# Kernel tuning notes

Measured on AMD Instinct MI355X. Metric: run time of the kernel, lower is better.

Reference implementation:

```python
import jax, jax.numpy as jnp
import numpy as np

G = 64          # graphs in batch
P = 31          # original nodes per graph
N_ORIG = G * P  # 1984 original nodes
N = N_ORIG + G  # 2048 total nodes (one virtual node per graph, appended at end)
D = 512         # hidden_dim
H = 8           # num_heads
DK = D // H     # per-head dim
FF = 2048       # dim_ff
L = 4           # num_layers
NF = 32         # num_node_features
MAX_SP = 100
MAX_DEG = 100


def setup_inputs() -> dict:
    key = jax.random.key(0)
    ks = jax.random.split(key, 24)
    s = 0.02
    return {
        "x": jax.random.normal(ks[0], (N_ORIG, NF), jnp.float32),
        "sp_matrix": jax.random.randint(ks[1], (N_ORIG, N_ORIG), 0, MAX_SP + 1, jnp.int32),
        "batch_ids": jnp.concatenate([
            jnp.repeat(jnp.arange(G, dtype=jnp.int32), P),
            jnp.arange(G, dtype=jnp.int32),
        ]),
        "degrees": jax.random.randint(ks[2], (N,), 0, MAX_DEG + 1, jnp.int32),
        "init_W": jax.random.normal(ks[3], (NF, D), jnp.float32) * s,
        "init_b": jnp.zeros((D,), jnp.float32),
        "cent_emb": jax.random.normal(ks[4], (MAX_DEG + 1, D), jnp.float32) * s,
        "dist_biases": jax.random.normal(ks[5], (MAX_SP + 2,), jnp.float32) * s,
        "virt_bias": jnp.zeros((), jnp.float32),
        "Wq": jax.random.normal(ks[6], (L, H, D, DK), jnp.float32) * s,
        "bq": jnp.zeros((L, H, DK), jnp.float32),
        "Wk": jax.random.normal(ks[7], (L, H, D, DK), jnp.float32) * s,
        "bk": jnp.zeros((L, H, DK), jnp.float32),
        "Wv": jax.random.normal(ks[8], (L, H, D, DK), jnp.float32) * s,
        "bv": jnp.zeros((L, H, DK), jnp.float32),
        "Wo": jax.random.normal(ks[9], (L, D, D), jnp.float32) * s,
        "bo": jnp.zeros((L, D), jnp.float32),
        "W1": jax.random.normal(ks[10], (L, D, FF), jnp.float32) * s,
        "b1": jnp.zeros((L, FF), jnp.float32),
        "W2": jax.random.normal(ks[11], (L, FF, D), jnp.float32) * s,
        "b2": jnp.zeros((L, D), jnp.float32),
    }


def _ln(h):
    # F.layer_norm with no affine params, eps=1e-5
    m = jnp.mean(h, axis=-1, keepdims=True)
    v = jnp.var(h, axis=-1, keepdims=True)
    return (h - m) / jnp.sqrt(v + 1e-5)


def reference(x, sp_matrix, batch_ids, degrees,
              init_W, init_b, cent_emb, dist_biases, virt_bias,
              Wq, bq, Wk, bk, Wv, bv, Wo, bo, W1, b1, W2, b2):
    same = batch_ids[:, None] == batch_ids[None, :]          # attention mask [N, N]
    is_virt = jnp.arange(N) >= N_ORIG

    # B matrix: fill with last distance bias (detached: torch uses .item()),
    # overwrite orig-orig block with sp-distance biases, virtual edges with
    # virt_bias, diagonal with dist_biases[0].
    fill = jax.lax.stop_gradient(dist_biases[-1])
    B = jnp.full((N, N), fill, dtype=jnp.float32)
    sp = jnp.minimum(sp_matrix, MAX_SP)
    B = B.at[:N_ORIG, :N_ORIG].set(dist_biases[sp])
    ve = (is_virt[:, None] ^ is_virt[None, :]) & same        # virt<->non-virt, same graph
    B = jnp.where(ve, virt_bias, B)
    diag = jnp.arange(N)
    B = B.at[diag, diag].set(dist_biases[0])

    # init projection, append virtual node states, add centrality encoding
    h = x @ init_W + init_b                                  # [N_ORIG, D]
    h = jnp.concatenate([h, jnp.zeros((G, D), h.dtype)], axis=0)   # [N, D]
    h = h + cent_emb[jnp.minimum(degrees, MAX_DEG)]

    scale = 1.0 / jnp.sqrt(jnp.float32(DK))
    for l in range(L):
        hn = _ln(h)
        Q = jnp.einsum('nd,hdk->hnk', hn, Wq[l]) + bq[l][:, None, :]   # [H, N, DK]
        K = jnp.einsum('nd,hdk->hnk', hn, Wk[l]) + bk[l][:, None, :]
        V = jnp.einsum('nd,hdk->hnk', hn, Wv[l]) + bv[l][:, None, :]
        logits = jnp.einsum('hik,hjk->hij', Q, K) * scale + B          # [H, N, N]
        logits = jnp.where(same, logits, -jnp.inf)
        w = jax.nn.softmax(logits, axis=-1)
        o = jnp.einsum('hij,hjk->hik', w, V)                           # [H, N, DK]
        o = jnp.transpose(o, (1, 0, 2)).reshape(N, D)                  # concat heads
        h = o @ Wo[l] + bo[l] + h                                      # residual
        hn2 = _ln(h)
        h = h + jax.nn.relu(hn2 @ W1[l] + b1[l]) @ W2[l] + b2[l]       # FFN residual

    return h[N_ORIG:]   # virtual node states, [G, D]
```

## Files before the change

### kernel.cpp

```cpp
#include <hip/hip_runtime.h>


#define NG   64
#define NP   31
#define NORI 1984
#define NT   2048
#define DIM  512
#define NHD  8
#define DKH  64
#define FFD  2048
#define NLAY 4
#define NFEA 32

typedef __attribute__((ext_vector_type(8))) short short8;
typedef __attribute__((ext_vector_type(4))) float floatx4;

__device__ __forceinline__ unsigned short f2bf(float f) {
    union { float f; unsigned u; } v; v.f = f;
    unsigned r = v.u + 0x7fffu + ((v.u >> 16) & 1u);
    return (unsigned short)(r >> 16);
}
__device__ __forceinline__ float bf2f(unsigned short u) {
    union { unsigned u; float f; } v; v.u = ((unsigned)u) << 16;
    return v.f;
}

__global__ __launch_bounds__(256) void prep_all(
    const float* __restrict__ x, const int* __restrict__ degrees,
    const float* __restrict__ init_W, const float* __restrict__ init_b,
    const float* __restrict__ cent_emb, float* __restrict__ h,
    const int* __restrict__ sp, const float* __restrict__ db,
    const float* __restrict__ virt_bias, float* __restrict__ Bg,
    const float* __restrict__ Wq, const float* __restrict__ Wk,
    const float* __restrict__ Wv, const float* __restrict__ bq,
    const float* __restrict__ bk, const float* __restrict__ bv,
    unsigned short* __restrict__ Wqkv_t, float* __restrict__ bqkv,
    const float* __restrict__ Wo, const float* __restrict__ W1,
    const float* __restrict__ W2, unsigned short* __restrict__ Wo_t,
    unsigned short* __restrict__ W1_t, unsigned short* __restrict__ W2_t)
{
    __shared__ float tl[32][33];
    int u = blockIdx.x;
    int tid = threadIdx.x;

    if (u < 2112) {
        int n = u;
        if (n >= NT) {
            int g = n - NT;
            float vb = virt_bias[0];
            for (int e = tid; e < 1024; e += 256) {
                int i = e >> 5, j = e & 31;
                float v;
                if (i == j) v = db[0];
                else if (i < NP && j < NP) {
                    int s = sp[(size_t)(g * NP + i) * NORI + g * NP + j];
                    v = db[s < 100 ? s : 100];
                } else v = vb;
                Bg[(size_t)g * 1024 + e] = v;
            }
            return;
        }
        float* xs = &tl[0][0];
        if (n < NORI && tid < NFEA) xs[tid] = x[(size_t)n * NFEA + tid];
        __syncthreads();
        int deg = degrees[n]; if (deg > 100) deg = 100;
        for (int d = tid; d < DIM; d += 256) {
            float v = cent_emb[(size_t)deg * DIM + d];
            if (n < NORI) {
                float acc = init_b[d];
                #pragma unroll
                for (int k = 0; k < NFEA; ++k) acc += xs[k] * init_W[(size_t)k * DIM + d];
                v += acc;
            }
            h[(size_t)n * DIM + d] = v;
        }
        return;
    }
    if (u < 5208) {
        int tile = u - 2112;
        if (tile >= 3072) {
            int idx = (tile - 3072) * 256 + tid;
            if (idx < NLAY * 1536) {
                int l = idx / 1536, c = idx % 1536;
                int which = c >> 9, cc = c & 511;
                const float* b = (which == 0) ? bq : (which == 1) ? bk : bv;
                bqkv[idx] = b[(size_t)l * 512 + cc];
            }
            return;
        }
        int slice = tile >> 5;
        int tloc = tile & 31;
        int dt = tloc >> 1, kt = tloc & 1;
        int l = slice / 24; int rem = slice % 24; int which = rem >> 3; int hh = rem & 7;
        const float* W = (which == 0) ? Wq : (which == 1) ? Wk : Wv;
        const float* in = W + (size_t)(l * 8 + hh) * DIM * DKH;
        int tr = tid >> 5, tc = tid & 31;
        #pragma unroll
        for (int pp = 0; pp < 4; ++pp)
            tl[tr + pp * 8][tc] = in[(size_t)(dt * 32 + tr + pp * 8) * DKH + kt * 32 + tc];
        __syncthreads();
        unsigned short* out = Wqkv_t +
            ((size_t)l * 1536 + which * 512 + hh * 64 + kt * 32) * DIM + dt * 32;
        #pragma unroll
        for (int pp = 0; pp < 4; ++pp)
            out[(size_t)(tr + pp * 8) * DIM + tc] = f2bf(tl[tc][tr + pp * 8]);
        return;
    }
    {
        int id = u - 5208;
        const float* in; unsigned short* outp; int R, C, l, rt, ct;
        if (id < 1024) {
            l = id >> 8; int t = id & 255; rt = t >> 4; ct = t & 15;
            in = Wo; outp = Wo_t; R = 512; C = 512;
        } else if (id < 5120) {
            int t2 = id - 1024; l = t2 >> 10; int t = t2 & 1023; rt = t >> 6; ct = t & 63;
            in = W1; outp = W1_t; R = 512; C = 2048;
        } else {
            int t2 = id - 5120; l = t2 >> 10; int t = t2 & 1023; rt = t >> 4; ct = t & 15;
            in = W2; outp = W2_t; R = 2048; C = 512;
        }
        const float* ip = in + (size_t)l * R * C;
        unsigned short* op = outp + (size_t)l * R * C;
        int r0 = rt * 32, c0 = ct * 32;
        int tr = tid >> 5, tc = tid & 31;
        #pragma unroll
        for (int pp = 0; pp < 4; ++pp)
            tl[tr + pp * 8][tc] = ip[(size_t)(r0 + tr + pp * 8) * C + c0 + tc];
        __syncthreads();
        #pragma unroll
        for (int pp = 0; pp < 4; ++pp)
            op[(size_t)(c0 + tr + pp * 8) * R + r0 + tc] = f2bf(tl[tc][tr + pp * 8]);
    }
}

__global__ __launch_bounds__(256) void layernorm_bf16(
    const float* __restrict__ in, unsigned short* __restrict__ out, int row0,
    float* __restrict__ fout)
{
    int n = row0 + blockIdx.x;
    int tid = threadIdx.x;
    const float* row = in + (size_t)n * DIM;
    float v0 = row[tid], v1 = row[tid + 256];
    float s = v0 + v1;
    float sq = v0 * v0 + v1 * v1;
    #pragma unroll
    for (int off = 32; off > 0; off >>= 1) {
        s  += __shfl_down(s, off);
        sq += __shfl_down(sq, off);
    }
    __shared__ float red[8];
    int wave = tid >> 6;
    if ((tid & 63) == 0) { red[wave] = s; red[4 + wave] = sq; }
    __syncthreads();
    float ts  = red[0] + red[1] + red[2] + red[3];
    float tsq = red[4] + red[5] + red[6] + red[7];
    float m   = ts * (1.0f / DIM);
    float var = tsq * (1.0f / DIM) - m * m;
    float inv = rsqrtf(var + 1e-5f);
    out[(size_t)n * DIM + tid]       = f2bf((v0 - m) * inv);
    out[(size_t)n * DIM + tid + 256] = f2bf((v1 - m) * inv);
    if (fout) {
        fout[(size_t)(n - row0) * DIM + tid]       = v0;
        fout[(size_t)(n - row0) * DIM + tid + 256] = v1;
    }
}

template<int SPLITK>
__global__ __launch_bounds__(256) void gemm64(
    const unsigned short* __restrict__ A, const unsigned short* __restrict__ Bt,
    const float* __restrict__ bias, void* __restrict__ out,
    int Nfull, int K, int moff, int flags, int P, int C, int orow)
{
    __shared__ __align__(16) unsigned short Asl[64 * 72];
    __shared__ __align__(16) unsigned short Bsl[64 * 72];
    int id = blockIdx.x;
    int by, bx, bz;
    if (P >= 8) {
        int xcd = id & 7, t = id >> 3, G = P >> 3;
        by = xcd + 8 * (t % G);
        int r2 = t / G;
        bx = r2 % C;
        bz = r2 / C;
    } else {
        by = id % P; int r2 = id / P; bx = r2 % C; bz = r2 / C;
    }
    int tid = threadIdx.x;
    int row0 = moff + by * 64, col0 = bx * 64;
    if ((flags & 4) && col0 < 512 && row0 < NORI) return;
    int kslice = K / SPLITK;
    int kbeg = bz * kslice;
    int wave = tid >> 6, lane = tid & 63;
    int quad = lane >> 4, m16 = lane & 15;
    int mw = (wave >> 1) * 32, nw = (wave & 1) * 32;
    floatx4 acc[2][2] = {};
    for (int k0 = kbeg; k0 < kbeg + kslice; k0 += 64) {
        #pragma unroll
        for (int p = 0; p < 2; ++p) {
            int idx = (p * 256 + tid) * 8;
            int r = idx >> 6, kk = idx & 63;
            *(float4*)(Asl + r * 72 + kk) =
                *(const float4*)(A + (size_t)(row0 + r) * K + k0 + kk);
            *(float4*)(Bsl + r * 72 + kk) =
                *(const float4*)(Bt + (size_t)(col0 + r) * K + k0 + kk);
        }
        __syncthreads();
        #pragma unroll
        for (int ks = 0; ks < 64; ks += 32) {
            short8 a[2], b[2];
            #pragma unroll
            for (int mi = 0; mi < 2; ++mi)
                a[mi] = *(const short8*)(Asl + (mw + mi * 16 + m16) * 72 + ks + quad * 8);
            #pragma unroll
            for (int ni = 0; ni < 2; ++ni)
                b[ni] = *(const short8*)(Bsl + (nw + ni * 16 + m16) * 72 + ks + quad * 8);
            #pragma unroll
            for (int mi = 0; mi < 2; ++mi)
                #pragma unroll
                for (int ni = 0; ni < 2; ++ni)
                    acc[mi][ni] = __builtin_amdgcn_mfma_f32_16x16x32_bf16(
                        a[mi], b[ni], acc[mi][ni], 0, 0, 0);
        }
        __syncthreads();
    }
    if (SPLITK == 1) {
        int do_relu = flags & 1, out_bf = flags & 2;
        #pragma unroll
        for (int mi = 0; mi < 2; ++mi) {
            #pragma unroll
            for (int ni = 0; ni < 2; ++ni) {
                int col = col0 + nw + ni * 16 + m16;
                float bval = bias[col];
                #pragma unroll
                for (int rr = 0; rr < 4; ++rr) {
                    int row = row0 + mw + mi * 16 + quad * 4 + rr;
                    float v = acc[mi][ni][rr] + bval;
                    if (do_relu) v = fmaxf(v, 0.0f);
                    if (out_bf) ((unsigned short*)out)[(size_t)(row - orow) * Nfull + col] = f2bf(v);
                    else        ((float*)out)[(size_t)(row - orow) * Nfull + col] = v;
                }
            }
        }
    } else {
        float* o = (float*)out;
        float bscale = (bz == 0) ? 1.0f : 0.0f;
        #pragma unroll
        for (int mi = 0; mi < 2; ++mi) {
            #pragma unroll
            for (int ni = 0; ni < 2; ++ni) {
                int col = col0 + nw + ni * 16 + m16;
                float bval = bias[col] * bscale;
                #pragma unroll
                for (int rr = 0; rr < 4; ++rr) {
                    int row = row0 + mw + mi * 16 + quad * 4 + rr;
                    atomicAdd(&o[(size_t)(row - orow) * Nfull + col],
                              acc[mi][ni][rr] + bval);
                }
            }
        }
    }
}

template<int SPLITK>
__global__ __launch_bounds__(256) void gemm128(
    const unsigned short* __restrict__ A, const unsigned short* __restrict__ Bt,
    const float* __restrict__ bias, void* __restrict__ out,
    int Nfull, int K, int flags, int P, int C)
{
    __shared__ __align__(16) unsigned short Asl[128 * 64];
    __shared__ __align__(16) unsigned short Bsl[128 * 64];
    int id = blockIdx.x;
    int xcd = id & 7, t = id >> 3, Gp = P >> 3;
    int by = xcd + 8 * (t % Gp);
    int r2 = t / Gp;
    int bx = r2 % C;
    int bz = r2 / C;
    int tid = threadIdx.x;
    int row0 = by * 128, col0 = bx * 128;
    if ((flags & 4) && col0 < 512 && row0 + 128 <= NORI) return;
    int kslice = K / SPLITK;
    int kbeg = bz * kslice;
    int wave = tid >> 6, lane = tid & 63;
    int quad = lane >> 4, m16 = lane & 15;
    int mw = (wave >> 1) * 64, nw = (wave & 1) * 64;
    int lr = lane >> 3;
    int srcswz = ((lane & 7) ^ lr) << 3;
    int rdswz = (m16 & 7) << 4;
    const unsigned short* Abase = A + (size_t)row0 * K;
    const unsigned short* Bbase = Bt + (size_t)col0 * K;
    floatx4 acc[4][4] = {};
    for (int k0 = kbeg; k0 < kbeg + kslice; k0 += 64) {
        #pragma unroll
        for (int p = 0; p < 4; ++p) {
            int chunk = wave * 4 + p;
            int r = chunk * 8 + lr;
            __builtin_amdgcn_global_load_lds(
                (const __attribute__((address_space(1))) unsigned int*)
                    (Abase + (size_t)r * K + k0 + srcswz),
                (__attribute__((address_space(3))) unsigned int*)
                    (Asl + chunk * 512 + lane * 8), 16, 0, 0);
            __builtin_amdgcn_global_load_lds(
                (const __attribute__((address_space(1))) unsigned int*)
                    (Bbase + (size_t)r * K + k0 + srcswz),
                (__attribute__((address_space(3))) unsigned int*)
                    (Bsl + chunk * 512 + lane * 8), 16, 0, 0);
        }
        __syncthreads();
        #pragma unroll
        for (int ks = 0; ks < 64; ks += 32) {
            short8 a[4], b[4];
            int cb = (ks + quad * 8) * 2;
            #pragma unroll
            for (int mi = 0; mi < 4; ++mi)
                a[mi] = *(const short8*)((const char*)Asl +
                        (mw + mi * 16 + m16) * 128 + (cb ^ rdswz));
            #pragma unroll
            for (int ni = 0; ni < 4; ++ni)
                b[ni] = *(const short8*)((const char*)Bsl +
                        (nw + ni * 16 + m16) * 128 + (cb ^ rdswz));
            #pragma unroll
            for (int mi = 0; mi < 4; ++mi)
                #pragma unroll
                for (int ni = 0; ni < 4; ++ni)
                    acc[mi][ni] = __builtin_amdgcn_mfma_f32_16x16x32_bf16(
                        a[mi], b[ni], acc[mi][ni], 0, 0, 0);
        }
        __syncthreads();
    }
    if (SPLITK == 1) {
        int do_relu = flags & 1, out_bf = flags & 2;
        #pragma unroll
        for (int mi = 0; mi < 4; ++mi) {
            #pragma unroll
            for (int ni = 0; ni < 4; ++ni) {
                int col = col0 + nw + ni * 16 + m16;
                float bval = bias[col];
                #pragma unroll
                for (int rr = 0; rr < 4; ++rr) {
                    int row = row0 + mw + mi * 16 + quad * 4 + rr;
                    float v = acc[mi][ni][rr] + bval;
                    if (do_relu) v = fmaxf(v, 0.0f);
                    if (out_bf) ((unsigned short*)out)[(size_t)row * Nfull + col] = f2bf(v);
                    else        ((float*)out)[(size_t)row * Nfull + col] = v;
                }
            }
        }
    } else {
        float* o = (float*)out;
        float bscale = (bz == 0) ? 1.0f : 0.0f;
        #pragma unroll
        for (int mi = 0; mi < 4; ++mi) {
            #pragma unroll
            for (int ni = 0; ni < 4; ++ni) {
                int col = col0 + nw + ni * 16 + m16;
                float bval = bias[col] * bscale;
                #pragma unroll
                for (int rr = 0; rr < 4; ++rr) {
                    int row = row0 + mw + mi * 16 + quad * 4 + rr;
                    atomicAdd(&o[(size_t)row * Nfull + col], acc[mi][ni][rr] + bval);
                }
            }
        }
    }
}

__global__ __launch_bounds__(256) void attention(
    const unsigned short* __restrict__ qkv,
    const float* __restrict__ Bg,
    unsigned short* __restrict__ O)
{
    int g = blockIdx.x >> 3;
    int hh = blockIdx.x & 7;
    __shared__ float Qs[32][65], Ks[32][65], Vs[32][65];
    __shared__ float S[32][33];
    int tid = threadIdx.x;
    int i = tid >> 3;
    int c0 = (tid & 7) * 8;
    int gn = (i < NP) ? g * NP + i : NORI + g;
    const unsigned short* base = qkv + (size_t)gn * 1536 + hh * DKH;
    short8 qv = *(const short8*)(base + c0);
    short8 kv = *(const short8*)(base + 512 + c0);
    short8 vv = *(const short8*)(base + 1024 + c0);
    #pragma unroll
    for (int j = 0; j < 8; ++j) {
        Qs[i][c0 + j] = bf2f((unsigned short)qv[j]);
        Ks[i][c0 + j] = bf2f((unsigned short)kv[j]);
        Vs[i][c0 + j] = bf2f((unsigned short)vv[j]);
    }
    __syncthreads();
    const float scale = 0.125f;
    #pragma unroll
    for (int e = 0; e < 4; ++e) {
        int idx = tid + e * 256;
        int si = idx >> 5, sj = idx & 31;
        float dot = 0.0f;
        #pragma unroll
        for (int k = 0; k < DKH; ++k) dot += Qs[si][k] * Ks[sj][k];
        S[si][sj] = dot * scale + Bg[(size_t)g * 1024 + si * 32 + sj];
    }
    __syncthreads();
    if (tid < 32) {
        float mx = -1e30f;
        #pragma unroll
        for (int j = 0; j < 32; ++j) mx = fmaxf(mx, S[tid][j]);
        float sum = 0.0f;
        #pragma unroll
        for (int j = 0; j < 32; ++j) { float e = __expf(S[tid][j] - mx); S[tid][j] = e; sum += e; }
        float inv = 1.0f / sum;
        #pragma unroll
        for (int j = 0; j < 32; ++j) S[tid][j] *= inv;
    }
    __syncthreads();
    short8 ov;
    #pragma unroll
    for (int cc = 0; cc < 8; ++cc) {
        float acc = 0.0f;
        #pragma unroll
        for (int j = 0; j < 32; ++j) acc += S[i][j] * Vs[j][c0 + cc];
        ov[cc] = (short)f2bf(acc);
    }
    *(short8*)(O + (size_t)gn * DIM + hh * DKH + c0) = ov;
}

__global__ __launch_bounds__(64) void attention_last(
    const unsigned short* __restrict__ qkv, const float* __restrict__ Bg,
    unsigned short* __restrict__ O)
{
    int g = blockIdx.x >> 3, hh = blockIdx.x & 7;
    __shared__ float Ks[32][65], Vs[32][65];
    __shared__ float Qs[64], P[32];
    int tid = threadIdx.x;
    int j = tid & 31, hf = tid >> 5;
    int gn = (j < NP) ? g * NP + j : NORI + g;
    const unsigned short* kb = qkv + (size_t)gn * 1536 + hh * DKH + 512 + hf * 32;
    #pragma unroll
    for (int c = 0; c < 32; c += 8) {
        short8 k8 = *(const short8*)(kb + c);
        short8 v8 = *(const short8*)(kb + 512 + c);
        #pragma unroll
        for (int t = 0; t < 8; ++t) {
            Ks[j][hf * 32 + c + t] = bf2f((unsigned short)k8[t]);
            Vs[j][hf * 32 + c + t] = bf2f((unsigned short)v8[t]);
        }
    }
    Qs[tid] = bf2f(qkv[(size_t)(NORI + g) * 1536 + hh * DKH + tid]);
    __syncthreads();
    float s;
    if (tid < 32) {
        float dot = 0.0f;
        #pragma unroll
        for (int k = 0; k < 64; ++k) dot += Qs[k] * Ks[tid][k];
        s = dot * 0.125f + Bg[(size_t)g * 1024 + 31 * 32 + tid];
    } else s = -1e30f;
    float mx = s;
    #pragma unroll
    for (int off = 32; off > 0; off >>= 1) mx = fmaxf(mx, __shfl_xor(mx, off));
    float e = (tid < 32) ? __expf(s - mx) : 0.0f;
    float sum = e;
    #pragma unroll
    for (int off = 32; off > 0; off >>= 1) sum += __shfl_xor(sum, off);
    if (tid < 32) P[tid] = e / sum;
    __syncthreads();
    float acc = 0.0f;
    #pragma unroll
    for (int jj = 0; jj < 32; ++jj) acc += P[jj] * Vs[jj][tid];
    O[(size_t)(NORI + g) * DIM + hh * DKH + tid] = f2bf(acc);
}

extern "C" void kernel_launch(void* const* d_in, const int* in_sizes, int n_in,
                              void* d_out, int out_size, void* d_ws, size_t ws_size,
                              hipStream_t stream)
{
    const float* x        = (const float*)d_in[0];
    const int*   sp       = (const int*)d_in[1];
    const int*   degrees  = (const int*)d_in[3];
    const float* init_W   = (const float*)d_in[4];
    const float* init_b   = (const float*)d_in[5];
    const float* cent_emb = (const float*)d_in[6];
    const float* db       = (const float*)d_in[7];
    const float* vbias    = (const float*)d_in[8];
    const float* Wq       = (const float*)d_in[9];
    const float* bq       = (const float*)d_in[10];
    const float* Wk       = (const float*)d_in[11];
    const float* bk       = (const float*)d_in[12];
    const float* Wv       = (const float*)d_in[13];
    const float* bv       = (const float*)d_in[14];
    const float* Wo       = (const float*)d_in[15];
    const float* bo       = (const float*)d_in[16];
    const float* W1       = (const float*)d_in[17];
    const float* b1       = (const float*)d_in[18];
    const float* W2       = (const float*)d_in[19];
    const float* b2       = (const float*)d_in[20];

    char* ws = (char*)d_ws;
    float*          h      = (float*)ws;          ws += (size_t)NT * DIM * 4;
    unsigned short* hn     = (unsigned short*)ws; ws += (size_t)NT * DIM * 2;
    unsigned short* o      = (unsigned short*)ws; ws += (size_t)NT * DIM * 2;
    unsigned short* qkv    = (unsigned short*)ws; ws += (size_t)NT * FFD * 2;
    float*          Bg     = (float*)ws;          ws += (size_t)NG * 1024 * 4;
    unsigned short* Wqkv_t = (unsigned short*)ws; ws += (size_t)NLAY * 1536 * DIM * 2;
    unsigned short* Wo_t   = (unsigned short*)ws; ws += (size_t)NLAY * DIM * DIM * 2;
    unsigned short* W1_t   = (unsigned short*)ws; ws += (size_t)NLAY * FFD * DIM * 2;
    unsigned short* W2_t   = (unsigned short*)ws; ws += (size_t)NLAY * DIM * FFD * 2;
    float*          bqkv   = (float*)ws;          ws += (size_t)NLAY * 1536 * 4;
    unsigned short* ffnb   = qkv;

    prep_all<<<14424, 256, 0, stream>>>(
        x, degrees, init_W, init_b, cent_emb, h, sp, db, vbias, Bg,
        Wq, Wk, Wv, bq, bk, bv, Wqkv_t, bqkv, Wo, W1, W2, Wo_t, W1_t, W2_t);

    for (int l = 0; l < NLAY - 1; ++l) {
        layernorm_bf16<<<NT, 256, 0, stream>>>(h, hn, 0, nullptr);
        gemm128<1><<<16 * 12, 256, 0, stream>>>(
            hn, Wqkv_t + (size_t)l * 1536 * DIM, bqkv + (size_t)l * 1536,
            qkv, 1536, DIM, 2, 16, 12);
        attention<<<NG * NHD, 256, 0, stream>>>(qkv, Bg, o);
        gemm128<2><<<16 * 4 * 2, 256, 0, stream>>>(
            o, Wo_t + (size_t)l * DIM * DIM, bo + (size_t)l * DIM,
            h, DIM, DIM, 0, 16, 4);
        layernorm_bf16<<<NT, 256, 0, stream>>>(h, hn, 0, nullptr);
        gemm128<1><<<16 * 16, 256, 0, stream>>>(
            hn, W1_t + (size_t)l * FFD * DIM, b1 + (size_t)l * FFD,
            ffnb, FFD, DIM, 3, 16, 16);
        gemm128<4><<<16 * 4 * 4, 256, 0, stream>>>(
            ffnb, W2_t + (size_t)l * DIM * FFD, b2 + (size_t)l * DIM,
            h, DIM, FFD, 0, 16, 4);
    }

    {
        int l = NLAY - 1;
        layernorm_bf16<<<NT, 256, 0, stream>>>(h, hn, 0, nullptr);
        gemm128<1><<<16 * 12, 256, 0, stream>>>(
            hn, Wqkv_t + (size_t)l * 1536 * DIM, bqkv + (size_t)l * 1536,
            qkv, 1536, DIM, 6, 16, 12);
        attention_last<<<NG * NHD, 64, 0, stream>>>(qkv, Bg, o);
        gemm64<8><<<1 * 8 * 8, 256, 0, stream>>>(
            o, Wo_t + (size_t)l * DIM * DIM, bo + (size_t)l * DIM,
            h, DIM, DIM, NORI, 0, 1, 8, 0);
        layernorm_bf16<<<NG, 256, 0, stream>>>(h, hn, NORI, (float*)d_out);
        gemm64<1><<<1 * 32, 256, 0, stream>>>(
            hn, W1_t + (size_t)l * FFD * DIM, b1 + (size_t)l * FFD,
            ffnb, FFD, DIM, NORI, 3, 1, 32, 0);
        gemm64<8><<<1 * 8 * 8, 256, 0, stream>>>(
            ffnb, W2_t + (size_t)l * DIM * FFD, b2 + (size_t)l * DIM,
            d_out, DIM, FFD, NORI, 0, 1, 8, NORI);
    }
}
```

Measured before the change: 452.5 us.

## Double-buffer LDS tiles in gemm128 and raise Wo split-K to four

The GEMM main loop now keeps two LDS buffers and issues the global-to-LDS loads for the next K tile before computing on the current one. Explicit vmcnt waits and raw barriers replace the previous syncthreads pair, so memory latency can overlap the MFMA work. Shared memory per block doubles, which may reduce occupancy. The Wo projection also moves from split-K 2 to 4, giving more blocks but more atomic adds into h.

```diff
diff --git a/kernel.cpp b/kernel.cpp
--- a/kernel.cpp
+++ b/kernel.cpp
@@ -260,14 +260,36 @@
     }
 }
 
+__device__ __forceinline__ void stage128(
+    const unsigned short* __restrict__ Abase, const unsigned short* __restrict__ Bbase,
+    int K, int k0, unsigned short* Asl, unsigned short* Bsl,
+    int wave, int lane, int lr, int scol)
+{
+    #pragma unroll
+    for (int p = 0; p < 4; ++p) {
+        int chunk = wave * 4 + p;
+        int r = chunk * 8 + lr;
+        __builtin_amdgcn_global_load_lds(
+            (const __attribute__((address_space(1))) unsigned int*)
+                (Abase + (size_t)r * K + k0 + scol),
+            (__attribute__((address_space(3))) unsigned int*)
+                (Asl + chunk * 512 + lane * 8), 16, 0, 0);
+        __builtin_amdgcn_global_load_lds(
+            (const __attribute__((address_space(1))) unsigned int*)
+                (Bbase + (size_t)r * K + k0 + scol),
+            (__attribute__((address_space(3))) unsigned int*)
+                (Bsl + chunk * 512 + lane * 8), 16, 0, 0);
+    }
+}
+
 template<int SPLITK>
 __global__ __launch_bounds__(256) void gemm128(
     const unsigned short* __restrict__ A, const unsigned short* __restrict__ Bt,
     const float* __restrict__ bias, void* __restrict__ out,
     int Nfull, int K, int flags, int P, int C)
 {
-    __shared__ __align__(16) unsigned short Asl[128 * 64];
-    __shared__ __align__(16) unsigned short Bsl[128 * 64];
+    __shared__ __align__(16) unsigned short Asl[2][128 * 64];
+    __shared__ __align__(16) unsigned short Bsl[2][128 * 64];
     int id = blockIdx.x;
     int xcd = id & 7, t = id >> 3, Gp = P >> 3;
     int by = xcd + 8 * (t % Gp);
@@ -279,44 +301,40 @@
     if ((flags & 4) && col0 < 512 && row0 + 128 <= NORI) return;
     int kslice = K / SPLITK;
     int kbeg = bz * kslice;
+    int nk = kslice >> 6;
     int wave = tid >> 6, lane = tid & 63;
     int quad = lane >> 4, m16 = lane & 15;
     int mw = (wave >> 1) * 64, nw = (wave & 1) * 64;
     int lr = lane >> 3;
-    int srcswz = ((lane & 7) ^ lr) << 3;
+    int scol = ((lane & 7) ^ lr) << 3;
     int rdswz = (m16 & 7) << 4;
     const unsigned short* Abase = A + (size_t)row0 * K;
     const unsigned short* Bbase = Bt + (size_t)col0 * K;
     floatx4 acc[4][4] = {};
-    for (int k0 = kbeg; k0 < kbeg + kslice; k0 += 64) {
-        #pragma unroll
-        for (int p = 0; p < 4; ++p) {
-            int chunk = wave * 4 + p;
-            int r = chunk * 8 + lr;
-            __builtin_amdgcn_global_load_lds(
-                (const __attribute__((address_space(1))) unsigned int*)
-                    (Abase + (size_t)r * K + k0 + srcswz),
-                (__attribute__((address_space(3))) unsigned int*)
-                    (Asl + chunk * 512 + lane * 8), 16, 0, 0);
-            __builtin_amdgcn_global_load_lds(
-                (const __attribute__((address_space(1))) unsigned int*)
-                    (Bbase + (size_t)r * K + k0 + srcswz),
-                (__attribute__((address_space(3))) unsigned int*)
-                    (Bsl + chunk * 512 + lane * 8), 16, 0, 0);
-        }
-        __syncthreads();
+
+    stage128(Abase, Bbase, K, kbeg, Asl[0], Bsl[0], wave, lane, lr, scol);
+    int cur = 0;
+    for (int i = 0; i < nk; ++i) {
+        if (i + 1 < nk) {
+            stage128(Abase, Bbase, K, kbeg + (i + 1) * 64,
+                     Asl[cur ^ 1], Bsl[cur ^ 1], wave, lane, lr, scol);
+            asm volatile("s_waitcnt vmcnt(8)" ::: "memory");
+        } else {
+            asm volatile("s_waitcnt vmcnt(0)" ::: "memory");
+        }
+        __builtin_amdgcn_s_barrier();
+        const char* Ac = (const char*)Asl[cur];
+        const char* Bc = (const char*)Bsl[cur];
         #pragma unroll
         for (int ks = 0; ks < 64; ks += 32) {
             short8 a[4], b[4];
             int cb = (ks + quad * 8) * 2;
             #pragma unroll
             for (int mi = 0; mi < 4; ++mi)
-                a[mi] = *(const short8*)((const char*)Asl +
-                        (mw + mi * 16 + m16) * 128 + (cb ^ rdswz));
+                a[mi] = *(const short8*)(Ac + (mw + mi * 16 + m16) * 128 + (cb ^ rdswz));
             #pragma unroll
             for (int ni = 0; ni < 4; ++ni)
-                b[ni] = *(const short8*)((const char*)Bsl +
-                        (nw + ni * 16 + m16) * 128 + (cb ^ rdswz));
+                b[ni] = *(const short8*)(Bc + (nw + ni * 16 + m16) * 128 + (cb ^ rdswz));
             #pragma unroll
             for (int mi = 0; mi < 4; ++mi)
                 #pragma unroll
@@ -324,7 +342,9 @@
                     acc[mi][ni] = __builtin_amdgcn_mfma_f32_16x16x32_bf16(
                         a[mi], b[ni], acc[mi][ni], 0, 0, 0);
         }
-        __syncthreads();
+        __builtin_amdgcn_s_barrier();
+        asm volatile("" ::: "memory");
+        cur ^= 1;
     }
     if (SPLITK == 1) {
         int do_relu = flags & 1, out_bf = flags & 2;
@@ -514,7 +534,7 @@
             hn, Wqkv_t + (size_t)l * 1536 * DIM, bqkv + (size_t)l * 1536,
             qkv, 1536, DIM, 2, 16, 12);
         attention<<<NG * NHD, 256, 0, stream>>>(qkv, Bg, o);
-        gemm128<2><<<16 * 4 * 2, 256, 0, stream>>>(
+        gemm128<4><<<16 * 4 * 4, 256, 0, stream>>>(
             o, Wo_t + (size_t)l * DIM * DIM, bo + (size_t)l * DIM,
             h, DIM, DIM, 0, 16, 4);
         layernorm_bf16<<<NT, 256, 0, stream>>>(h, hn, 0, nullptr);
```

After: 451.7 us. Within noise of the previous version (-0.2%).
